# Kernel optimization log

Hardware: AMD Instinct MI355X
Metric: run time of the kernel (lower is better)

The kernel has to match this reference:

```python
import jax, jax.numpy as jnp
import numpy as np

EPS = 1e-7
NUM_HEADS = 16

def _ln(x, g, b):
    m = jnp.mean(x, -1, keepdims=True)
    v = jnp.var(x, -1, keepdims=True)
    return (x - m) * jax.lax.rsqrt(v + EPS) * g + b

def _gelu(x):
    return jax.nn.gelu(x, approximate=False)  # torch nn.GELU default = exact erf

def _attn(x, qkv_w, qkv_b, pw, pb):
    B, N, C = x.shape
    D = C // NUM_HEADS
    qkv = (x @ qkv_w.T + qkv_b).reshape(B, N, 3, NUM_HEADS, D).transpose(2, 0, 3, 1, 4)
    q, k, v = qkv[0], qkv[1], qkv[2]
    a = jax.nn.softmax(jnp.einsum('bhnd,bhmd->bhnm', q, k) * (D ** -0.5), axis=-1)
    o = jnp.einsum('bhnm,bhmd->bhnd', a, v).transpose(0, 2, 1, 3).reshape(B, N, C)
    return o @ pw.T + pb

def _gcn(x, w, b, adj):
    # x: (B,C,J); w: (C*K,C) 1x1 conv, then einsum 'nkctv,kvw->nctw' with t==1
    K = adj.shape[0]
    B, C, J = x.shape
    y = jnp.einsum('bcj,oc->boj', x, w) + b[None, :, None]
    y = y.reshape(B, K, C, J)
    return jnp.einsum('bkcv,kvw->bcw', y, adj)

def _mlp(x, w1, b1, w2, b2):
    return _gelu(_gelu(x @ w1.T + b1) @ w2.T + b2)

def _lrsc(x, adj, l1g, l1b, l2g, l2b, g1w, g1b, g2w, g2b, m1w, m1b, m2w, m2b):
    x = x.transpose(0, 2, 1)                       # (B,C,J)
    res = x
    xn = _ln(x, l1g, l1b)                          # LayerNorm over J
    x = res + _mlp(xn, m1w, m1b, m2w, m2b) + _gcn(xn, g1w, g1b, adj)
    x = _ln(x.transpose(0, 2, 1), l2g, l2b).transpose(0, 2, 1)  # LayerNorm over C
    res = x
    x = res + _mlp(x, m1w, m1b, m2w, m2b) + _gcn(x, g2w, g2b, adj)
    return x.transpose(0, 2, 1)                    # (B,J,C)

def _gkpc(x, lg, lb, q1w, q1b, p1w, p1b, q2w, q2b, p2w, p2b):
    x = x + _attn(_ln(x, lg, lb), q1w, q1b, p1w, p1b)
    return _attn(_ln(x, lg, lb), q2w, q2b, p2w, p2b)  # note: no residual on second attn

def _forward(x, adj, ln1_g, ln1_b, ln2_g, ln2_b, gcn1_w, gcn1_b, gcn2_w, gcn2_b,
             mlp1_w1, mlp1_b1, mlp1_w2, mlp1_b2, attn_ln_g, attn_ln_b,
             qkv1_w, qkv1_b, proj1_w, proj1_b, qkv2_w, qkv2_b, proj2_w, proj2_b,
             tn_g, tn_b):
    L = ln1_g.shape[0]
    for i in range(L):
        # GG_ACM/RR_ACM/LCM are published as identity -> both 0.3/0.7 mixes equal x + gelu(x)
        xin = x + _gelu(x)
        x5 = _gkpc(xin, attn_ln_g[i], attn_ln_b[i], qkv1_w[i], qkv1_b[i],
                   proj1_w[i], proj1_b[i], qkv2_w[i], qkv2_b[i], proj2_w[i], proj2_b[i])
        x7 = _lrsc(xin, adj, ln1_g[i], ln1_b[i], ln2_g[i], ln2_b[i],
                   gcn1_w[i], gcn1_b[i], gcn2_w[i], gcn2_b[i],
                   mlp1_w1[i], mlp1_b1[i], mlp1_w2[i], mlp1_b2[i])
        x = x + x5 + x7
    return _ln(x, tn_g, tn_b)

def setup_inputs():
    B, V, C, K, L = 2048, 17, 512, 3, 3
    s = 0.05
    ks = jax.random.split(jax.random.key(0), 12)
    rn = lambda k, sh: jax.random.normal(k, sh, jnp.float32) * s
    return dict(
        x=jax.random.normal(ks[0], (B, V, C), jnp.float32),
        adj=jax.random.uniform(ks[1], (K, V, V), dtype=jnp.float32),
        ln1_g=jnp.ones((L, V), jnp.float32), ln1_b=jnp.zeros((L, V), jnp.float32),
        ln2_g=jnp.ones((L, C), jnp.float32), ln2_b=jnp.zeros((L, C), jnp.float32),
        gcn1_w=rn(ks[2], (L, C * K, C)), gcn1_b=jnp.zeros((L, C * K), jnp.float32),
        gcn2_w=rn(ks[3], (L, C * K, C)), gcn2_b=jnp.zeros((L, C * K), jnp.float32),
        mlp1_w1=rn(ks[4], (L, C, V)), mlp1_b1=jnp.zeros((L, C), jnp.float32),
        mlp1_w2=rn(ks[5], (L, V, C)), mlp1_b2=jnp.zeros((L, V), jnp.float32),
        attn_ln_g=jnp.ones((L, C), jnp.float32), attn_ln_b=jnp.zeros((L, C), jnp.float32),
        qkv1_w=rn(ks[6], (L, 3 * C, C)), qkv1_b=jnp.zeros((L, 3 * C), jnp.float32),
        proj1_w=rn(ks[7], (L, C, C)), proj1_b=jnp.zeros((L, C), jnp.float32),
        qkv2_w=rn(ks[8], (L, 3 * C, C)), qkv2_b=jnp.zeros((L, 3 * C), jnp.float32),
        proj2_w=rn(ks[9], (L, C, C)), proj2_b=jnp.zeros((L, C), jnp.float32),
        tn_g=jnp.ones((C,), jnp.float32), tn_b=jnp.zeros((C,), jnp.float32),
    )

def reference(x, adj, ln1_g, ln1_b, ln2_g, ln2_b, gcn1_w, gcn1_b, gcn2_w, gcn2_b,
              mlp1_w1, mlp1_b1, mlp1_w2, mlp1_b2, attn_ln_g, attn_ln_b,
              qkv1_w, qkv1_b, proj1_w, proj1_b, qkv2_w, qkv2_b, proj2_w, proj2_b,
              tn_g, tn_b):
    return _forward(x, adj, ln1_g, ln1_b, ln2_g, ln2_b, gcn1_w, gcn1_b, gcn2_w, gcn2_b,
                    mlp1_w1, mlp1_b1, mlp1_w2, mlp1_b2, attn_ln_g, attn_ln_b,
                    qkv1_w, qkv1_b, proj1_w, proj1_b, qkv2_w, qkv2_b, proj2_w, proj2_b,
                    tn_g, tn_b)
```

## Files before the change

### kernel.cpp

```cpp
#include <hip/hip_runtime.h>
#include <hip/hip_bf16.h>
#include <math.h>

#define Bn 2048
#define Vn 17
#define Cn 512
static const size_t NE = (size_t)Bn * Vn * Cn;
#define MROWS (Bn * Vn)

typedef __attribute__((ext_vector_type(8))) short bf16x8;
typedef __attribute__((ext_vector_type(4))) short bf16x4;
typedef __attribute__((ext_vector_type(4))) float f32x4;
typedef __attribute__((ext_vector_type(2))) unsigned int u32x2;
typedef unsigned short u16;

__device__ __forceinline__ float u2f(u16 u) { return __uint_as_float(((unsigned)u) << 16); }
__device__ __forceinline__ u16 f2u(float f) {
    unsigned u = __float_as_uint(f);
    return (u16)((u + 0x7fffu + ((u >> 16) & 1u)) >> 16);
}
__device__ __forceinline__ float gelu_f(float x) {
    return 0.5f * x * (1.0f + erff(x * 0.70710678118654752f));
}
__device__ __forceinline__ float exp2_raw(float x) {
    float r; asm("v_exp_f32 %0, %1" : "=v"(r) : "v"(x)); return r;
}
__device__ __forceinline__ float gelu_fast(float x) {
    float b = x * fmaf(x * x, -0.10294348f, -2.30220820f);
    return x * __builtin_amdgcn_rcpf(1.0f + exp2_raw(b));
}
__device__ __forceinline__ unsigned cvtpk(float lo, float hi) {
    unsigned r; asm("v_cvt_pk_bf16_f32 %0, %1, %2" : "=v"(r) : "v"(lo), "v"(hi)); return r;
}
__device__ __forceinline__ bf16x4 gelupk(f32x4 v) {
    u32x2 t = {cvtpk(gelu_fast(v[0]), gelu_fast(v[1])), cvtpk(gelu_fast(v[2]), gelu_fast(v[3]))};
    return __builtin_bit_cast(bf16x4, t);
}
__device__ __forceinline__ f32x4 mfma16(bf16x4 a, bf16x4 b, f32x4 c) {
    asm("v_mfma_f32_16x16x16_bf16 %0, %1, %2, %0" : "+v"(c) : "v"(a), "v"(b));
    return c;
}
__device__ __forceinline__ void gload16(const u16* g, u16* l) {
    __builtin_amdgcn_global_load_lds((const __attribute__((address_space(1))) void*)g,
                                     (__attribute__((address_space(3))) void*)l, 16, 0, 0);
}

__global__ void k_diag(float* __restrict__ o, float v, int n) {
    int i = blockIdx.x * 256 + threadIdx.x;
    if (i < n) o[i] = v;
}

__global__ void k_f2b(const float4* __restrict__ s, ushort4* __restrict__ d, int n4) {
    int i = blockIdx.x * 256 + threadIdx.x;
    if (i >= n4) return;
    float4 v = s[i];
    ushort4 o = {f2u(v.x), f2u(v.y), f2u(v.z), f2u(v.w)};
    d[i] = o;
}

__global__ void k_mpad(const float* __restrict__ W1, const float* __restrict__ W2,
                       u16* __restrict__ W1p, u16* __restrict__ W2p) {
    int t = blockIdx.x * 256 + threadIdx.x;
    if (t < 512 * 32) {
        int o = t >> 5, j = t & 31;
        W1p[t] = (j < 17) ? f2u(W1[o * 17 + j]) : (u16)0;
    } else {
        int t2 = t - 512 * 32;
        int w = t2 >> 9;
        W2p[t2] = (w < 17) ? f2u(W2[t2]) : (u16)0;
    }
}

__global__ void k_xingelu(const float* __restrict__ X, u16* __restrict__ O, int n8) {
    int i = blockIdx.x * 256 + threadIdx.x;
    if (i >= n8) return;
    float4 a = *(const float4*)(X + (size_t)i * 8);
    float4 b = *(const float4*)(X + (size_t)i * 8 + 4);
    float v[8] = {a.x, a.y, a.z, a.w, b.x, b.y, b.z, b.w};
    bf16x8 r;
#pragma unroll
    for (int k = 0; k < 8; k++) r[k] = f2u(v[k] + gelu_f(v[k]));
    *(bf16x8*)(O + (size_t)i * 8) = r;
}

template <int F32IO>
__global__ __launch_bounds__(256) void k_ln_c(const void* __restrict__ Xv,
                                              const float* __restrict__ g,
                                              const float* __restrict__ bt,
                                              void* __restrict__ Ov, int nrows) {
    int row = blockIdx.x * 4 + (threadIdx.x >> 6);
    if (row >= nrows) return;
    int lane = threadIdx.x & 63;
    float vv[8];
    if (F32IO) {
        const float* xp = (const float*)Xv + (size_t)row * Cn + lane * 8;
        float4 v0 = *(const float4*)xp, v1 = *(const float4*)(xp + 4);
        vv[0] = v0.x; vv[1] = v0.y; vv[2] = v0.z; vv[3] = v0.w;
        vv[4] = v1.x; vv[5] = v1.y; vv[6] = v1.z; vv[7] = v1.w;
    } else {
        bf16x8 h = *(const bf16x8*)((const u16*)Xv + (size_t)row * Cn + lane * 8);
#pragma unroll
        for (int k = 0; k < 8; k++) vv[k] = u2f((u16)h[k]);
    }
    float s = 0.f, q = 0.f;
#pragma unroll
    for (int k = 0; k < 8; k++) { s += vv[k]; q = fmaf(vv[k], vv[k], q); }
#pragma unroll
    for (int o = 32; o; o >>= 1) { s += __shfl_xor(s, o); q += __shfl_xor(q, o); }
    float mean = s * (1.f / Cn);
    float var = q * (1.f / Cn) - mean * mean;
    float inv = 1.f / sqrtf(var + 1e-7f);
    int cb = lane * 8;
    if (F32IO) {
        float r[8];
#pragma unroll
        for (int k = 0; k < 8; k++) r[k] = (vv[k] - mean) * inv * g[cb + k] + bt[cb + k];
        float* op = (float*)Ov + (size_t)row * Cn + cb;
        *(float4*)op = make_float4(r[0], r[1], r[2], r[3]);
        *(float4*)(op + 4) = make_float4(r[4], r[5], r[6], r[7]);
    } else {
        bf16x8 r;
#pragma unroll
        for (int k = 0; k < 8; k++) r[k] = f2u((vv[k] - mean) * inv * g[cb + k] + bt[cb + k]);
        *(bf16x8*)((u16*)Ov + (size_t)row * Cn + cb) = r;
    }
}

__global__ __launch_bounds__(256) void k_ln_j(const u16* __restrict__ X,
                                              const float* __restrict__ g,
                                              const float* __restrict__ bt,
                                              u16* __restrict__ O) {
    int idx = blockIdx.x * 256 + threadIdx.x;
    int b = idx >> 9, c = idx & 511;
    const u16* xp = X + (size_t)b * Vn * Cn + c;
    float v[Vn];
    float s = 0.f;
#pragma unroll
    for (int j = 0; j < Vn; j++) { v[j] = u2f(xp[(size_t)j * Cn]); s += v[j]; }
    float mean = s * (1.f / Vn);
    float q = 0.f;
#pragma unroll
    for (int j = 0; j < Vn; j++) { float d = v[j] - mean; q = fmaf(d, d, q); }
    float inv = 1.f / sqrtf(q * (1.f / Vn) + 1e-7f);
    u16* op = O + (size_t)b * Vn * Cn + c;
#pragma unroll
    for (int j = 0; j < Vn; j++) op[(size_t)j * Cn] = f2u((v[j] - mean) * inv * g[j] + bt[j]);
}

template <int REMAP, int EPI>
__global__ __launch_bounds__(256) void k_gemm(const u16* __restrict__ A, const u16* __restrict__ W,
                                              const float* __restrict__ bias, u16* __restrict__ OutB,
                                              const u16* __restrict__ Res, float* __restrict__ Xf,
                                              int hbase, int shift) {
    constexpr int NT = REMAP ? 6 : 8;
    const int K = 512;
    int wave = threadIdx.x >> 6, lane = threadIdx.x & 63;
    int m0 = blockIdx.x * 128 + wave * 32;
    int nbase = blockIdx.y * (16 * NT);
    int r16 = lane & 15, kq = lane >> 4;
    int ld = REMAP ? (3 << shift) : 512;

    const u16* wp[NT];
    int wrow[NT];
#pragma unroll
    for (int nt = 0; nt < NT; nt++) {
        int n = nbase + nt * 16 + r16;
        int wr;
        if (REMAP) {
            int s = n >> shift, off = n & ((1 << shift) - 1);
            wr = (s << 9) + hbase + off;
        } else wr = n;
        wrow[nt] = wr;
        wp[nt] = W + (size_t)wr * K + kq * 8;
    }
    f32x4 acc[2][NT];
#pragma unroll
    for (int i = 0; i < 2; i++)
#pragma unroll
        for (int nt = 0; nt < NT; nt++) acc[i][nt] = (f32x4){0.f, 0.f, 0.f, 0.f};

    const u16* ap = A + (size_t)(m0 + r16) * K + kq * 8;
    for (int k0 = 0; k0 < K; k0 += 32) {
        bf16x8 a0 = *(const bf16x8*)(ap + k0);
        bf16x8 a1 = *(const bf16x8*)(ap + (size_t)16 * K + k0);
#pragma unroll
        for (int nt = 0; nt < NT; nt++) {
            bf16x8 bf = *(const bf16x8*)(wp[nt] + k0);
            acc[0][nt] = __builtin_amdgcn_mfma_f32_16x16x32_bf16(a0, bf, acc[0][nt], 0, 0, 0);
            acc[1][nt] = __builtin_amdgcn_mfma_f32_16x16x32_bf16(a1, bf, acc[1][nt], 0, 0, 0);
        }
    }
#pragma unroll
    for (int nt = 0; nt < NT; nt++) {
        float bv = bias[wrow[nt]];
        int n = nbase + nt * 16 + r16;
#pragma unroll
        for (int i = 0; i < 2; i++) {
#pragma unroll
            for (int r = 0; r < 4; r++) {
                size_t mb = (size_t)(m0 + i * 16 + kq * 4 + r);
                float v = acc[i][nt][r] + bv;
                if (EPI == 0) OutB[mb * ld + n] = f2u(v);
                else if (EPI == 1) { size_t o = mb * 512 + n; OutB[o] = f2u(v + u2f(Res[o])); }
                else { size_t o = mb * 512 + n; Xf[o] += v; }
            }
        }
    }
}

template <int EPI, int NY>
__global__ __launch_bounds__(256) void k_gemm2(const u16* __restrict__ A, const u16* __restrict__ W,
                                               const float* __restrict__ bias, u16* __restrict__ OutB,
                                               const u16* __restrict__ Res, float* __restrict__ Xf,
                                               int N) {
    __shared__ u16 As[128 * 64];
    __shared__ u16 Bs[128 * 64];
    const int K = 512;
    int tid = threadIdx.x;
    int wave = tid >> 6, lane = tid & 63;
    int cpx = gridDim.x >> 3;
    int bid = blockIdx.x;
    int swz = (bid & 7) * cpx + (bid >> 3);
    int m0 = (swz / NY) * 128, n0 = (swz % NY) * 128;
    int r16 = lane & 15, kq = lane >> 4;

    int srow = wave << 2;
    int lrow = lane >> 3;
    int lcol = (lane & 7) * 8;

    f32x4 acc[2][8];
#pragma unroll
    for (int i = 0; i < 2; i++)
#pragma unroll
        for (int j = 0; j < 8; j++) acc[i][j] = (f32x4){0.f, 0.f, 0.f, 0.f};

    const u16* aT = As + (wave * 32 + r16) * 64 + kq * 8;
    const u16* bT = Bs + r16 * 64 + kq * 8;

    for (int k0 = 0; k0 < K; k0 += 64) {
#pragma unroll
        for (int i = 0; i < 4; i++) {
            int rows = (srow + i) * 8 + lrow;
            gload16(A + (size_t)(m0 + rows) * K + k0 + lcol, (u16*)As + (srow + i) * 512);
            gload16(W + (size_t)(n0 + rows) * K + k0 + lcol, (u16*)Bs + (srow + i) * 512);
        }
        __syncthreads();
#pragma unroll
        for (int kk = 0; kk < 64; kk += 32) {
            bf16x8 af0 = *(const bf16x8*)(aT + kk);
            bf16x8 af1 = *(const bf16x8*)(aT + 16 * 64 + kk);
#pragma unroll
            for (int nt = 0; nt < 8; nt++) {
                bf16x8 bf = *(const bf16x8*)(bT + nt * 16 * 64 + kk);
                acc[0][nt] = __builtin_amdgcn_mfma_f32_16x16x32_bf16(af0, bf, acc[0][nt], 0, 0, 0);
                acc[1][nt] = __builtin_amdgcn_mfma_f32_16x16x32_bf16(af1, bf, acc[1][nt], 0, 0, 0);
            }
        }
        __syncthreads();
    }

    int mw = m0 + wave * 32;
#pragma unroll
    for (int nt = 0; nt < 8; nt++) {
        int n = n0 + nt * 16 + r16;
        float bv = bias[n];
#pragma unroll
        for (int i = 0; i < 2; i++) {
#pragma unroll
            for (int r = 0; r < 4; r++) {
                size_t mb = (size_t)(mw + i * 16 + kq * 4 + r);
                size_t o = mb * N + n;
                float v = acc[i][nt][r] + bv;
                if (EPI == 0) OutB[o] = f2u(v);
                else if (EPI == 1) OutB[o] = f2u(v + u2f(Res[o]));
                else Xf[o] += v;
            }
        }
    }
}

__global__ __launch_bounds__(256) void k_attn(const u16* __restrict__ Y, u16* __restrict__ T,
                                              int shift, int hgbase, int l2ch) {
    int wv = threadIdx.x >> 6, lane = threadIdx.x & 63;
    if (lane >= 34) return;
    int gw = blockIdx.x * 4 + wv;
    int which = (lane >= 17) ? 1 : 0;
    int j = lane - which * 17;
    int pid = gw * 2 + which;
    int b = pid >> l2ch;
    int hl = pid & ((1 << l2ch) - 1);
    int CW = 1 << shift;
    int row3 = 3 << shift;

    const u16* qb = Y + (size_t)(b * Vn + j) * row3 + hl * 32;
    float q[32];
#pragma unroll
    for (int d0 = 0; d0 < 32; d0 += 8) {
        bf16x8 h = *(const bf16x8*)(qb + d0);
#pragma unroll
        for (int d = 0; d < 8; d++) q[d0 + d] = u2f((u16)h[d]);
    }
    float sc[Vn];
    float mx = -1e30f;
#pragma unroll
    for (int kk = 0; kk < Vn; kk++) {
        const u16* kb = Y + (size_t)(b * Vn + kk) * row3 + CW + hl * 32;
        float s = 0.f;
#pragma unroll
        for (int d0 = 0; d0 < 32; d0 += 8) {
            bf16x8 h = *(const bf16x8*)(kb + d0);
#pragma unroll
            for (int d = 0; d < 8; d++) s = fmaf(q[d0 + d], u2f((u16)h[d]), s);
        }
        s *= 0.1767766952966369f;
        sc[kk] = s;
        mx = fmaxf(mx, s);
    }
    float sum = 0.f;
#pragma unroll
    for (int kk = 0; kk < Vn; kk++) { sc[kk] = __expf(sc[kk] - mx); sum += sc[kk]; }
    float inv = 1.f / sum;
    float o[32];
#pragma unroll
    for (int d = 0; d < 32; d++) o[d] = 0.f;
#pragma unroll
    for (int kk = 0; kk < Vn; kk++) {
        const u16* vb = Y + (size_t)(b * Vn + kk) * row3 + 2 * CW + hl * 32;
        float p = sc[kk] * inv;
#pragma unroll
        for (int d0 = 0; d0 < 32; d0 += 8) {
            bf16x8 h = *(const bf16x8*)(vb + d0);
#pragma unroll
            for (int d = 0; d < 8; d++) o[d0 + d] = fmaf(p, u2f((u16)h[d]), o[d0 + d]);
        }
    }
    u16* op = T + (size_t)(b * Vn + j) * Cn + hgbase + hl * 32;
#pragma unroll
    for (int d0 = 0; d0 < 32; d0 += 8) {
        bf16x8 r;
#pragma unroll
        for (int d = 0; d < 8; d++) r[d] = f2u(o[d0 + d]);
        *(bf16x8*)(op + d0) = r;
    }
}

template <int MODE>
__global__ __launch_bounds__(256) void k_agg(const u16* __restrict__ Y, const float* __restrict__ Adj,
                                             const u16* __restrict__ aux1, const u16* __restrict__ aux2,
                                             u16* __restrict__ OutB, float* __restrict__ Xf,
                                             int cbase, int shift) {
    __shared__ float adj_s[3][Vn][Vn];
    for (int t = threadIdx.x; t < 3 * Vn * Vn; t += 256) {
        int k = t / (Vn * Vn), r = t - k * Vn * Vn;
        adj_s[k][r / Vn][r % Vn] = Adj[t];
    }
    __syncthreads();
    int CW = 1 << shift;
    int idx = blockIdx.x * 256 + threadIdx.x;
    int b = idx >> shift, co = idx & (CW - 1);
    int c = cbase + co;
    int row3 = 3 << shift;
    float acc[Vn];
#pragma unroll
    for (int w = 0; w < Vn; w++) acc[w] = 0.f;
    const u16* yb = Y + (size_t)b * Vn * row3 + co;
#pragma unroll
    for (int k = 0; k < 3; k++)
#pragma unroll
        for (int v = 0; v < Vn; v++) {
            float y = u2f(yb[(size_t)v * row3 + k * CW]);
#pragma unroll
            for (int w = 0; w < Vn; w++) acc[w] = fmaf(y, adj_s[k][v][w], acc[w]);
        }
    size_t rb = (size_t)(b * Vn) * Cn + c;
#pragma unroll
    for (int w = 0; w < Vn; w++) {
        size_t o = rb + (size_t)w * Cn;
        float val = acc[w] + u2f(aux1[o]) + u2f(aux2[o]);
        if (MODE == 0) OutB[o] = f2u(val);
        else Xf[o] += val;
    }
}

__global__ __launch_bounds__(512) void k_mlp(const u16* __restrict__ X,
                                             const u16* __restrict__ W1p, const float* __restrict__ B1,
                                             const u16* __restrict__ W2p, const float* __restrict__ B2,
                                             u16* __restrict__ O) {
    __shared__ u16 Xs[256 * 40];
    __shared__ float B1s[512];
    int b = blockIdx.x >> 1;
    int cbase = (blockIdx.x & 1) << 8;
    int tid = threadIdx.x;

    for (int i = tid; i < 256 * 40 / 8; i += 512) ((float4*)Xs)[i] = make_float4(0.f, 0.f, 0.f, 0.f);
    if (tid < 128) ((float4*)B1s)[tid] = ((const float4*)B1)[tid];
    __syncthreads();
    const u16* xb = X + (size_t)b * (Vn * Cn) + cbase;
    for (int i = tid; i < 17 * 256; i += 512) {
        int j = i >> 8, c = i & 255;
        Xs[c * 40 + j] = xb[j * Cn + c];
    }
    __syncthreads();

    int wave = tid >> 6, lane = tid & 63;
    int r16 = lane & 15, kq = lane >> 4;
    int crow = wave * 32;

    bf16x8 xf0 = *(const bf16x8*)(Xs + (crow + r16) * 40 + kq * 8);
    bf16x8 xf1 = *(const bf16x8*)(Xs + (crow + 16 + r16) * 40 + kq * 8);

    f32x4 acc2[2][2];
#pragma unroll
    for (int i = 0; i < 2; i++)
#pragma unroll
        for (int j = 0; j < 2; j++) acc2[i][j] = (f32x4){0.f, 0.f, 0.f, 0.f};

    for (int s = 0; s < 16; s++) {
        const u16* w1p = W1p + ((s * 32 + r16) << 5) + kq * 8;
        bf16x8 af0 = *(const bf16x8*)w1p;
        bf16x8 af1 = *(const bf16x8*)(w1p + 16 * 32);
        f32x4 bi0 = *(const f32x4*)(B1s + s * 32 + kq * 4);
        f32x4 bi1 = *(const f32x4*)(B1s + s * 32 + 16 + kq * 4);
        f32x4 a00 = __builtin_amdgcn_mfma_f32_16x16x32_bf16(af0, xf0, bi0, 0, 0, 0);
        f32x4 a01 = __builtin_amdgcn_mfma_f32_16x16x32_bf16(af0, xf1, bi0, 0, 0, 0);
        f32x4 a10 = __builtin_amdgcn_mfma_f32_16x16x32_bf16(af1, xf0, bi1, 0, 0, 0);
        f32x4 a11 = __builtin_amdgcn_mfma_f32_16x16x32_bf16(af1, xf1, bi1, 0, 0, 0);
        bf16x4 p00 = gelupk(a00);
        bf16x4 p01 = gelupk(a01);
        bf16x4 p10 = gelupk(a10);
        bf16x4 p11 = gelupk(a11);
        const u16* w2p = W2p + (size_t)r16 * 512 + s * 32 + kq * 4;
        bf16x4 wb00 = *(const bf16x4*)(w2p);
        bf16x4 wb01 = *(const bf16x4*)(w2p + 16);
        bf16x4 wb10 = *(const bf16x4*)(w2p + 16 * 512);
        bf16x4 wb11 = *(const bf16x4*)(w2p + 16 * 512 + 16);
        acc2[0][0] = mfma16(p00, wb00, acc2[0][0]);
        acc2[0][0] = mfma16(p10, wb01, acc2[0][0]);
        acc2[1][0] = mfma16(p01, wb00, acc2[1][0]);
        acc2[1][0] = mfma16(p11, wb01, acc2[1][0]);
        acc2[0][1] = mfma16(p00, wb10, acc2[0][1]);
        acc2[0][1] = mfma16(p10, wb11, acc2[0][1]);
        acc2[1][1] = mfma16(p01, wb10, acc2[1][1]);
        acc2[1][1] = mfma16(p11, wb11, acc2[1][1]);
    }

    u16* ob = O + (size_t)b * (Vn * Cn) + cbase;
    float bb0 = B2[r16];
#pragma unroll
    for (int cg = 0; cg < 2; cg++) {
        int cl = crow + cg * 16 + kq * 4;
        f32x4 v = acc2[cg][0];
        uint2 pk = make_uint2(cvtpk(gelu_fast(v[0] + bb0), gelu_fast(v[1] + bb0)),
                              cvtpk(gelu_fast(v[2] + bb0), gelu_fast(v[3] + bb0)));
        *(uint2*)(ob + (size_t)r16 * Cn + cl) = pk;
        if (r16 == 0) {
            float bb1 = B2[16];
            f32x4 w = acc2[cg][1];
            uint2 pk1 = make_uint2(cvtpk(gelu_fast(w[0] + bb1), gelu_fast(w[1] + bb1)),
                                   cvtpk(gelu_fast(w[2] + bb1), gelu_fast(w[3] + bb1)));
            *(uint2*)(ob + (size_t)16 * Cn + cl) = pk1;
        }
    }
}

extern "C" void kernel_launch(void* const* d_in, const int* in_sizes, int n_in,
                              void* d_out, int out_size, void* d_ws, size_t ws_size,
                              hipStream_t stream) {
    (void)in_sizes; (void)n_in; (void)out_size;
    typedef const float* fp;
    fp x_in = (fp)d_in[0];
    fp adj = (fp)d_in[1];
    fp ln1_g = (fp)d_in[2], ln1_b = (fp)d_in[3];
    fp ln2_g = (fp)d_in[4], ln2_b = (fp)d_in[5];
    fp gcn1_w = (fp)d_in[6], gcn1_b = (fp)d_in[7];
    fp gcn2_w = (fp)d_in[8], gcn2_b = (fp)d_in[9];
    fp m1w = (fp)d_in[10], m1b = (fp)d_in[11];
    fp m2w = (fp)d_in[12], m2b = (fp)d_in[13];
    fp aln_g = (fp)d_in[14], aln_b = (fp)d_in[15];
    fp qkv1_w = (fp)d_in[16], qkv1_b = (fp)d_in[17];
    fp p1w = (fp)d_in[18], p1b = (fp)d_in[19];
    fp qkv2_w = (fp)d_in[20], qkv2_b = (fp)d_in[21];
    fp p2w = (fp)d_in[22], p2b = (fp)d_in[23];
    fp tn_g = (fp)d_in[24], tn_b = (fp)d_in[25];

    const size_t NE2 = NE * 2;
    const size_t WSCR_SZ = (size_t)1536 * 512 * 2;
    const size_t MPAD_SZ = (size_t)(512 * 32 + 32 * 512) * 2;

    int CH = 0;
    for (int ch = 16; ch >= 1; ch >>= 1) {
        size_t need = 3 * NE2 + WSCR_SZ + MPAD_SZ + (size_t)MROWS * 96 * ch * 2 + 1024;
        if (need <= ws_size) { CH = ch; break; }
    }
    if (!CH) {
        k_diag<<<(int)((NE + 255) / 256), 256, 0, stream>>>((float*)d_out, (float)ws_size, (int)NE);
        return;
    }
    const int l2ch = __builtin_ctz(CH);
    const int shift = 5 + l2ch;
    const int NCH = 16 / CH;
    const bool FAST = (CH == 16);

    char* p = (char*)d_ws;
    u16* XIN = (u16*)p;  p += NE2;
    u16* T1 = (u16*)p;   p += NE2;
    u16* T2 = (u16*)p;   p += NE2;
    u16* YCH = (u16*)p;  p += (size_t)MROWS * 96 * CH * 2;
    u16* WSCR = (u16*)p; p += WSCR_SZ;
    u16* MPAD1 = (u16*)p;
    u16* MPAD2 = MPAD1 + 512 * 32;

    float* X = (float*)d_out;
    hipMemcpyAsync(X, x_in, NE * 4, hipMemcpyDeviceToDevice, stream);

    const int G8 = (int)(NE / 8 / 256);
    const int GLN = MROWS / 4;
    const int GBC = Bn * Cn / 256;
    const int GATT = (Bn << l2ch) / 8;
    const int GAGG = (Bn << shift) / 256;
    const dim3 GEMM_C(MROWS / 128, CH);
    const dim3 GEMM_P(MROWS / 128, 4);
    const int CV_QKV = (int)(1536 * 512 / 4 / 256);
    const int CV_P = (int)(512 * 512 / 4 / 256);
    const int GQF = (MROWS / 128) * 12;
    const int GPF = (MROWS / 128) * 4;

    for (int i = 0; i < 3; i++) {
        fp q1w = qkv1_w + (size_t)i * 1536 * 512, q1b = qkv1_b + i * 1536;
        fp q2w = qkv2_w + (size_t)i * 1536 * 512, q2b = qkv2_b + i * 1536;
        fp g1w = gcn1_w + (size_t)i * 1536 * 512, g1b = gcn1_b + i * 1536;
        fp g2w = gcn2_w + (size_t)i * 1536 * 512, g2b = gcn2_b + i * 1536;
        fp pw1 = p1w + (size_t)i * 512 * 512, pb1 = p1b + i * Cn;
        fp pw2 = p2w + (size_t)i * 512 * 512, pb2 = p2b + i * Cn;
        fp alg = aln_g + i * Cn, alb = aln_b + i * Cn;
        fp l1g = ln1_g + i * Vn, l1b_ = ln1_b + i * Vn;
        fp l2g = ln2_g + i * Cn, l2b_ = ln2_b + i * Cn;
        fp w1 = m1w + (size_t)i * Cn * Vn, b1 = m1b + i * Cn;
        fp w2 = m2w + (size_t)i * Vn * Cn, b2 = m2b + i * Vn;

        k_xingelu<<<G8, 256, 0, stream>>>(X, XIN, (int)(NE / 8));
        k_mpad<<<128, 256, 0, stream>>>(w1, w2, MPAD1, MPAD2);

        k_ln_c<0><<<GLN, 256, 0, stream>>>(XIN, alg, alb, T1, MROWS);
        k_f2b<<<CV_QKV, 256, 0, stream>>>((const float4*)q1w, (ushort4*)WSCR, 1536 * 512 / 4);
        if (FAST) {
            k_gemm2<0, 12><<<GQF, 256, 0, stream>>>(T1, WSCR, q1b, YCH, nullptr, nullptr, 1536);
            k_attn<<<GATT, 256, 0, stream>>>(YCH, T2, shift, 0, l2ch);
        } else {
            for (int hg = 0; hg < NCH; hg++) {
                k_gemm<1, 0><<<GEMM_C, 256, 0, stream>>>(T1, WSCR, q1b, YCH, nullptr, nullptr, hg << shift, shift);
                k_attn<<<GATT, 256, 0, stream>>>(YCH, T2, shift, hg << shift, l2ch);
            }
        }
        k_f2b<<<CV_P, 256, 0, stream>>>((const float4*)pw1, (ushort4*)WSCR, 512 * 512 / 4);
        if (FAST) k_gemm2<1, 4><<<GPF, 256, 0, stream>>>(T2, WSCR, pb1, T1, XIN, nullptr, 512);
        else k_gemm<0, 1><<<GEMM_P, 256, 0, stream>>>(T2, WSCR, pb1, T1, XIN, nullptr, 0, 0);
        k_ln_c<0><<<GLN, 256, 0, stream>>>(T1, alg, alb, T2, MROWS);
        k_f2b<<<CV_QKV, 256, 0, stream>>>((const float4*)q2w, (ushort4*)WSCR, 1536 * 512 / 4);
        if (FAST) {
            k_gemm2<0, 12><<<GQF, 256, 0, stream>>>(T2, WSCR, q2b, YCH, nullptr, nullptr, 1536);
            k_attn<<<GATT, 256, 0, stream>>>(YCH, T1, shift, 0, l2ch);
        } else {
            for (int hg = 0; hg < NCH; hg++) {
                k_gemm<1, 0><<<GEMM_C, 256, 0, stream>>>(T2, WSCR, q2b, YCH, nullptr, nullptr, hg << shift, shift);
                k_attn<<<GATT, 256, 0, stream>>>(YCH, T1, shift, hg << shift, l2ch);
            }
        }
        k_f2b<<<CV_P, 256, 0, stream>>>((const float4*)pw2, (ushort4*)WSCR, 512 * 512 / 4);
        if (FAST) k_gemm2<2, 4><<<GPF, 256, 0, stream>>>(T1, WSCR, pb2, nullptr, nullptr, X, 512);
        else k_gemm<0, 2><<<GEMM_P, 256, 0, stream>>>(T1, WSCR, pb2, nullptr, nullptr, X, 0, 0);

        k_ln_j<<<GBC, 256, 0, stream>>>(XIN, l1g, l1b_, T1);
        k_mlp<<<Bn * 2, 512, 0, stream>>>(T1, MPAD1, b1, MPAD2, b2, T2);
        k_f2b<<<CV_QKV, 256, 0, stream>>>((const float4*)g1w, (ushort4*)WSCR, 1536 * 512 / 4);
        if (FAST) {
            k_gemm2<0, 12><<<GQF, 256, 0, stream>>>(T1, WSCR, g1b, YCH, nullptr, nullptr, 1536);
            k_agg<0><<<GAGG, 256, 0, stream>>>(YCH, adj, XIN, T2, XIN, nullptr, 0, shift);
        } else {
            for (int cc = 0; cc < NCH; cc++) {
                k_gemm<1, 0><<<GEMM_C, 256, 0, stream>>>(T1, WSCR, g1b, YCH, nullptr, nullptr, cc << shift, shift);
                k_agg<0><<<GAGG, 256, 0, stream>>>(YCH, adj, XIN, T2, XIN, nullptr, cc << shift, shift);
            }
        }
        k_ln_c<0><<<GLN, 256, 0, stream>>>(XIN, l2g, l2b_, T1, MROWS);
        k_mlp<<<Bn * 2, 512, 0, stream>>>(T1, MPAD1, b1, MPAD2, b2, T2);
        k_f2b<<<CV_QKV, 256, 0, stream>>>((const float4*)g2w, (ushort4*)WSCR, 1536 * 512 / 4);
        if (FAST) {
            k_gemm2<0, 12><<<GQF, 256, 0, stream>>>(T1, WSCR, g2b, YCH, nullptr, nullptr, 1536);
            k_agg<1><<<GAGG, 256, 0, stream>>>(YCH, adj, T1, T2, nullptr, X, 0, shift);
        } else {
            for (int cc = 0; cc < NCH; cc++) {
                k_gemm<1, 0><<<GEMM_C, 256, 0, stream>>>(T1, WSCR, g2b, YCH, nullptr, nullptr, cc << shift, shift);
                k_agg<1><<<GAGG, 256, 0, stream>>>(YCH, adj, T1, T2, nullptr, X, cc << shift, shift);
            }
        }
    }

    k_ln_c<1><<<GLN, 256, 0, stream>>>(X, tn_g, tn_b, X, MROWS);
}
```

Before: 4.397 ms.

## Pre-convert all layer weights upfront and stage MLP hidden via LDS

When the workspace is large enough, all per-layer weights are converted to bf16 in one batch at the start instead of re-converting into a shared scratch before every GEMM. This removes many small conversion launches from the per-layer sequence. The MLP kernel now writes GELU outputs to an LDS buffer and reloads them as 16x16x32 MFMA operands, replacing the 16x16x16 inline-asm MFMAs. Inline-asm exp and bf16 packing are swapped for builtins. The cost is extra workspace and extra LDS per block.

Result: faster. 3.774 ms (-14.2%).

```diff
diff --git a/kernel.cpp b/kernel.cpp
--- a/kernel.cpp
+++ b/kernel.cpp
@@ -9,9 +9,7 @@
 #define MROWS (Bn * Vn)
 
 typedef __attribute__((ext_vector_type(8))) short bf16x8;
-typedef __attribute__((ext_vector_type(4))) short bf16x4;
 typedef __attribute__((ext_vector_type(4))) float f32x4;
-typedef __attribute__((ext_vector_type(2))) unsigned int u32x2;
 typedef unsigned short u16;
 
 __device__ __forceinline__ float u2f(u16 u) { return __uint_as_float(((unsigned)u) << 16); }
@@ -22,23 +20,22 @@
 __device__ __forceinline__ float gelu_f(float x) {
     return 0.5f * x * (1.0f + erff(x * 0.70710678118654752f));
 }
-__device__ __forceinline__ float exp2_raw(float x) {
-    float r; asm("v_exp_f32 %0, %1" : "=v"(r) : "v"(x)); return r;
+__device__ __forceinline__ float exp2f_fast(float b) {
+#if __has_builtin(__builtin_amdgcn_exp2f)
+    return __builtin_amdgcn_exp2f(b);
+#else
+    return __expf(b * 0.69314718056f);
+#endif
 }
 __device__ __forceinline__ float gelu_fast(float x) {
     float b = x * fmaf(x * x, -0.10294348f, -2.30220820f);
-    return x * __builtin_amdgcn_rcpf(1.0f + exp2_raw(b));
-}
-__device__ __forceinline__ unsigned cvtpk(float lo, float hi) {
-    unsigned r; asm("v_cvt_pk_bf16_f32 %0, %1, %2" : "=v"(r) : "v"(lo), "v"(hi)); return r;
-}
-__device__ __forceinline__ bf16x4 gelupk(f32x4 v) {
-    u32x2 t = {cvtpk(gelu_fast(v[0]), gelu_fast(v[1])), cvtpk(gelu_fast(v[2]), gelu_fast(v[3]))};
-    return __builtin_bit_cast(bf16x4, t);
-}
-__device__ __forceinline__ f32x4 mfma16(bf16x4 a, bf16x4 b, f32x4 c) {
-    asm("v_mfma_f32_16x16x16_bf16 %0, %1, %2, %0" : "+v"(c) : "v"(a), "v"(b));
-    return c;
+    return x * __builtin_amdgcn_rcpf(1.0f + exp2f_fast(b));
+}
+__device__ __forceinline__ unsigned pk2(float lo, float hi) {
+    __hip_bfloat162 h = __float22bfloat162_rn(make_float2(lo, hi));
+    unsigned r;
+    __builtin_memcpy(&r, &h, 4);
+    return r;
 }
 __device__ __forceinline__ void gload16(const u16* g, u16* l) {
     __builtin_amdgcn_global_load_lds((const __attribute__((address_space(1))) void*)g,
@@ -387,6 +384,7 @@
                                              const u16* __restrict__ W2p, const float* __restrict__ B2,
                                              u16* __restrict__ O) {
     __shared__ u16 Xs[256 * 40];
+    __shared__ u16 Hs[256 * 40];
     __shared__ float B1s[512];
     int b = blockIdx.x >> 1;
     int cbase = (blockIdx.x & 1) << 8;
@@ -414,6 +412,8 @@
     for (int i = 0; i < 2; i++)
 #pragma unroll
         for (int j = 0; j < 2; j++) acc2[i][j] = (f32x4){0.f, 0.f, 0.f, 0.f};
+
+    const u16* hs0 = Hs + (crow + r16) * 40 + kq * 8;
 
     for (int s = 0; s < 16; s++) {
         const u16* w1p = W1p + ((s * 32 + r16) << 5) + kq * 8;
@@ -425,40 +425,44 @@
         f32x4 a01 = __builtin_amdgcn_mfma_f32_16x16x32_bf16(af0, xf1, bi0, 0, 0, 0);
         f32x4 a10 = __builtin_amdgcn_mfma_f32_16x16x32_bf16(af1, xf0, bi1, 0, 0, 0);
         f32x4 a11 = __builtin_amdgcn_mfma_f32_16x16x32_bf16(af1, xf1, bi1, 0, 0, 0);
-        bf16x4 p00 = gelupk(a00);
-        bf16x4 p01 = gelupk(a01);
-        bf16x4 p10 = gelupk(a10);
-        bf16x4 p11 = gelupk(a11);
-        const u16* w2p = W2p + (size_t)r16 * 512 + s * 32 + kq * 4;
-        bf16x4 wb00 = *(const bf16x4*)(w2p);
-        bf16x4 wb01 = *(const bf16x4*)(w2p + 16);
-        bf16x4 wb10 = *(const bf16x4*)(w2p + 16 * 512);
-        bf16x4 wb11 = *(const bf16x4*)(w2p + 16 * 512 + 16);
-        acc2[0][0] = mfma16(p00, wb00, acc2[0][0]);
-        acc2[0][0] = mfma16(p10, wb01, acc2[0][0]);
-        acc2[1][0] = mfma16(p01, wb00, acc2[1][0]);
-        acc2[1][0] = mfma16(p11, wb01, acc2[1][0]);
-        acc2[0][1] = mfma16(p00, wb10, acc2[0][1]);
-        acc2[0][1] = mfma16(p10, wb11, acc2[0][1]);
-        acc2[1][1] = mfma16(p01, wb10, acc2[1][1]);
-        acc2[1][1] = mfma16(p11, wb11, acc2[1][1]);
+#define STORE_H(ACC, NT, OT)                                                             \
+        {                                                                                 \
+            unsigned g0 = pk2(gelu_fast(ACC[0]), gelu_fast(ACC[1]));                      \
+            unsigned g1 = pk2(gelu_fast(ACC[2]), gelu_fast(ACC[3]));                      \
+            *(uint2*)(Hs + (crow + NT * 16 + r16) * 40 + OT * 16 + kq * 4) =              \
+                make_uint2(g0, g1);                                                       \
+        }
+        STORE_H(a00, 0, 0)
+        STORE_H(a01, 1, 0)
+        STORE_H(a10, 0, 1)
+        STORE_H(a11, 1, 1)
+#undef STORE_H
+        __builtin_amdgcn_sched_barrier(0);
+        bf16x8 h0 = *(const bf16x8*)hs0;
+        bf16x8 h1 = *(const bf16x8*)(hs0 + 16 * 40);
+        const u16* w2p = W2p + s * 32 + kq * 8;
+        bf16x8 wf0 = *(const bf16x8*)(w2p + r16 * 512);
+        bf16x8 wf1 = *(const bf16x8*)(w2p + 16 * 512);
+        acc2[0][0] = __builtin_amdgcn_mfma_f32_16x16x32_bf16(h0, wf0, acc2[0][0], 0, 0, 0);
+        acc2[0][1] = __builtin_amdgcn_mfma_f32_16x16x32_bf16(h0, wf1, acc2[0][1], 0, 0, 0);
+        acc2[1][0] = __builtin_amdgcn_mfma_f32_16x16x32_bf16(h1, wf0, acc2[1][0], 0, 0, 0);
+        acc2[1][1] = __builtin_amdgcn_mfma_f32_16x16x32_bf16(h1, wf1, acc2[1][1], 0, 0, 0);
     }
 
     u16* ob = O + (size_t)b * (Vn * Cn) + cbase;
-    float bb0 = B2[r16];
-#pragma unroll
-    for (int cg = 0; cg < 2; cg++) {
-        int cl = crow + cg * 16 + kq * 4;
-        f32x4 v = acc2[cg][0];
-        uint2 pk = make_uint2(cvtpk(gelu_fast(v[0] + bb0), gelu_fast(v[1] + bb0)),
-                              cvtpk(gelu_fast(v[2] + bb0), gelu_fast(v[3] + bb0)));
-        *(uint2*)(ob + (size_t)r16 * Cn + cl) = pk;
-        if (r16 == 0) {
-            float bb1 = B2[16];
-            f32x4 w = acc2[cg][1];
-            uint2 pk1 = make_uint2(cvtpk(gelu_fast(w[0] + bb1), gelu_fast(w[1] + bb1)),
-                                   cvtpk(gelu_fast(w[2] + bb1), gelu_fast(w[3] + bb1)));
-            *(uint2*)(ob + (size_t)16 * Cn + cl) = pk1;
+#pragma unroll
+    for (int nt = 0; nt < 2; nt++) {
+        int cl = crow + nt * 16 + kq * 4;
+#pragma unroll
+        for (int n2 = 0; n2 < 2; n2++) {
+            int w = n2 * 16 + r16;
+            if (w < 17) {
+                float bb = B2[w];
+                f32x4 v = acc2[nt][n2];
+                uint2 pk = make_uint2(pk2(gelu_fast(v[0] + bb), gelu_fast(v[1] + bb)),
+                                      pk2(gelu_fast(v[2] + bb), gelu_fast(v[3] + bb)));
+                *(uint2*)(ob + (size_t)w * Cn + cl) = pk;
+            }
         }
     }
 }
@@ -484,13 +488,22 @@
     fp tn_g = (fp)d_in[24], tn_b = (fp)d_in[25];
 
     const size_t NE2 = NE * 2;
+    const size_t YCH16 = (size_t)MROWS * 96 * 16 * 2;
+    const size_t SZ_QKV3 = (size_t)3 * 1536 * 512;
+    const size_t SZ_P3 = (size_t)3 * 512 * 512;
+    const size_t MPADL = (size_t)(512 * 32 + 32 * 512);
+    const size_t POOLB = (4 * SZ_QKV3 + 2 * SZ_P3 + 3 * MPADL) * 2;
     const size_t WSCR_SZ = (size_t)1536 * 512 * 2;
-    const size_t MPAD_SZ = (size_t)(512 * 32 + 32 * 512) * 2;
-
+    const size_t MPAD_SZ = MPADL * 2;
+
+    bool FULLW = false;
     int CH = 0;
-    for (int ch = 16; ch >= 1; ch >>= 1) {
-        size_t need = 3 * NE2 + WSCR_SZ + MPAD_SZ + (size_t)MROWS * 96 * ch * 2 + 1024;
-        if (need <= ws_size) { CH = ch; break; }
+    if (3 * NE2 + YCH16 + POOLB + 1024 <= ws_size) { FULLW = true; CH = 16; }
+    else {
+        for (int ch = 16; ch >= 1; ch >>= 1) {
+            size_t need = 3 * NE2 + WSCR_SZ + MPAD_SZ + (size_t)MROWS * 96 * ch * 2 + 1024;
+            if (need <= ws_size) { CH = ch; break; }
+        }
     }
     if (!CH) {
         k_diag<<<(int)((NE + 255) / 256), 256, 0, stream>>>((float*)d_out, (float)ws_size, (int)NE);
@@ -506,12 +519,37 @@
     u16* T1 = (u16*)p;   p += NE2;
     u16* T2 = (u16*)p;   p += NE2;
     u16* YCH = (u16*)p;  p += (size_t)MROWS * 96 * CH * 2;
-    u16* WSCR = (u16*)p; p += WSCR_SZ;
-    u16* MPAD1 = (u16*)p;
-    u16* MPAD2 = MPAD1 + 512 * 32;
+    u16 *WQ1 = nullptr, *WQ2 = nullptr, *WG1 = nullptr, *WG2 = nullptr,
+        *WP1 = nullptr, *WP2 = nullptr, *MP1 = nullptr, *MP2 = nullptr, *WSCR = nullptr;
+    if (FULLW) {
+        WQ1 = (u16*)p; p += SZ_QKV3 * 2;
+        WQ2 = (u16*)p; p += SZ_QKV3 * 2;
+        WG1 = (u16*)p; p += SZ_QKV3 * 2;
+        WG2 = (u16*)p; p += SZ_QKV3 * 2;
+        WP1 = (u16*)p; p += SZ_P3 * 2;
+        WP2 = (u16*)p; p += SZ_P3 * 2;
+        MP1 = (u16*)p; p += 3 * 16384 * 2;
+        MP2 = (u16*)p; p += 3 * 16384 * 2;
+    } else {
+        WSCR = (u16*)p; p += WSCR_SZ;
+        MP1 = (u16*)p;  p += 16384 * 2;
+        MP2 = (u16*)p;
+    }
 
     float* X = (float*)d_out;
-    hipMemcpyAsync(X, x_in, NE * 4, hipMemcpyDeviceToDevice, stream);
+    (void)hipMemcpyAsync(X, x_in, NE * 4, hipMemcpyDeviceToDevice, stream);
+
+    if (FULLW) {
+        k_f2b<<<2304, 256, 0, stream>>>((const float4*)qkv1_w, (ushort4*)WQ1, (int)(SZ_QKV3 / 4));
+        k_f2b<<<2304, 256, 0, stream>>>((const float4*)qkv2_w, (ushort4*)WQ2, (int)(SZ_QKV3 / 4));
+        k_f2b<<<2304, 256, 0, stream>>>((const float4*)gcn1_w, (ushort4*)WG1, (int)(SZ_QKV3 / 4));
+        k_f2b<<<2304, 256, 0, stream>>>((const float4*)gcn2_w, (ushort4*)WG2, (int)(SZ_QKV3 / 4));
+        k_f2b<<<768, 256, 0, stream>>>((const float4*)p1w, (ushort4*)WP1, (int)(SZ_P3 / 4));
+        k_f2b<<<768, 256, 0, stream>>>((const float4*)p2w, (ushort4*)WP2, (int)(SZ_P3 / 4));
+        for (int l = 0; l < 3; l++)
+            k_mpad<<<128, 256, 0, stream>>>(m1w + (size_t)l * Cn * Vn, m2w + (size_t)l * Vn * Cn,
+                                            MP1 + l * 16384, MP2 + l * 16384);
+    }
 
     const int G8 = (int)(NE / 8 / 256);
     const int GLN = MROWS / 4;
@@ -538,13 +576,22 @@
         fp w1 = m1w + (size_t)i * Cn * Vn, b1 = m1b + i * Cn;
         fp w2 = m2w + (size_t)i * Vn * Cn, b2 = m2b + i * Vn;
 
+        const u16* wq1p = FULLW ? WQ1 + (size_t)i * 1536 * 512 : WSCR;
+        const u16* wq2p = FULLW ? WQ2 + (size_t)i * 1536 * 512 : WSCR;
+        const u16* wg1p = FULLW ? WG1 + (size_t)i * 1536 * 512 : WSCR;
+        const u16* wg2p = FULLW ? WG2 + (size_t)i * 1536 * 512 : WSCR;
+        const u16* wp1p = FULLW ? WP1 + (size_t)i * 512 * 512 : WSCR;
+        const u16* wp2p = FULLW ? WP2 + (size_t)i * 512 * 512 : WSCR;
+        const u16* mp1 = FULLW ? MP1 + i * 16384 : MP1;
+        const u16* mp2 = FULLW ? MP2 + i * 16384 : MP2;
+
         k_xingelu<<<G8, 256, 0, stream>>>(X, XIN, (int)(NE / 8));
-        k_mpad<<<128, 256, 0, stream>>>(w1, w2, MPAD1, MPAD2);
+        if (!FULLW) k_mpad<<<128, 256, 0, stream>>>(w1, w2, (u16*)mp1, (u16*)mp2);
 
         k_ln_c<0><<<GLN, 256, 0, stream>>>(XIN, alg, alb, T1, MROWS);
-        k_f2b<<<CV_QKV, 256, 0, stream>>>((const float4*)q1w, (ushort4*)WSCR, 1536 * 512 / 4);
+        if (!FULLW) k_f2b<<<CV_QKV, 256, 0, stream>>>((const float4*)q1w, (ushort4*)WSCR, 1536 * 512 / 4);
         if (FAST) {
-            k_gemm2<0, 12><<<GQF, 256, 0, stream>>>(T1, WSCR, q1b, YCH, nullptr, nullptr, 1536);
+            k_gemm2<0, 12><<<GQF, 256, 0, stream>>>(T1, wq1p, q1b, YCH, nullptr, nullptr, 1536);
             k_attn<<<GATT, 256, 0, stream>>>(YCH, T2, shift, 0, l2ch);
         } else {
             for (int hg = 0; hg < NCH; hg++) {
@@ -552,13 +599,13 @@
                 k_attn<<<GATT, 256, 0, stream>>>(YCH, T2, shift, hg << shift, l2ch);
             }
         }
-        k_f2b<<<CV_P, 256, 0, stream>>>((const float4*)pw1, (ushort4*)WSCR, 512 * 512 / 4);
-        if (FAST) k_gemm2<1, 4><<<GPF, 256, 0, stream>>>(T2, WSCR, pb1, T1, XIN, nullptr, 512);
+        if (!FULLW) k_f2b<<<CV_P, 256, 0, stream>>>((const float4*)pw1, (ushort4*)WSCR, 512 * 512 / 4);
+        if (FAST) k_gemm2<1, 4><<<GPF, 256, 0, stream>>>(T2, wp1p, pb1, T1, XIN, nullptr, 512);
         else k_gemm<0, 1><<<GEMM_P, 256, 0, stream>>>(T2, WSCR, pb1, T1, XIN, nullptr, 0, 0);
         k_ln_c<0><<<GLN, 256, 0, stream>>>(T1, alg, alb, T2, MROWS);
-        k_f2b<<<CV_QKV, 256, 0, stream>>>((const float4*)q2w, (ushort4*)WSCR, 1536 * 512 / 4);
+        if (!FULLW) k_f2b<<<CV_QKV, 256, 0, stream>>>((const float4*)q2w, (ushort4*)WSCR, 1536 * 512 / 4);
         if (FAST) {
-            k_gemm2<0, 12><<<GQF, 256, 0, stream>>>(T2, WSCR, q2b, YCH, nullptr, nullptr, 1536);
+            k_gemm2<0, 12><<<GQF, 256, 0, stream>>>(T2, wq2p, q2b, YCH, nullptr, nullptr, 1536);
             k_attn<<<GATT, 256, 0, stream>>>(YCH, T1, shift, 0, l2ch);
         } else {
             for (int hg = 0; hg < NCH; hg++) {
@@ -566,15 +613,15 @@
                 k_attn<<<GATT, 256, 0, stream>>>(YCH, T1, shift, hg << shift, l2ch);
             }
         }
-        k_f2b<<<CV_P, 256, 0, stream>>>((const float4*)pw2, (ushort4*)WSCR, 512 * 512 / 4);
-        if (FAST) k_gemm2<2, 4><<<GPF, 256, 0, stream>>>(T1, WSCR, pb2, nullptr, nullptr, X, 512);
+        if (!FULLW) k_f2b<<<CV_P, 256, 0, stream>>>((const float4*)pw2, (ushort4*)WSCR, 512 * 512 / 4);
+        if (FAST) k_gemm2<2, 4><<<GPF, 256, 0, stream>>>(T1, wp2p, pb2, nullptr, nullptr, X, 512);
         else k_gemm<0, 2><<<GEMM_P, 256, 0, stream>>>(T1, WSCR, pb2, nullptr, nullptr, X, 0, 0);
 
         k_ln_j<<<GBC, 256, 0, stream>>>(XIN, l1g, l1b_, T1);
-        k_mlp<<<Bn * 2, 512, 0, stream>>>(T1, MPAD1, b1, MPAD2, b2, T2);
-        k_f2b<<<CV_QKV, 256, 0, stream>>>((const float4*)g1w, (ushort4*)WSCR, 1536 * 512 / 4);
+        k_mlp<<<Bn * 2, 512, 0, stream>>>(T1, mp1, b1, mp2, b2, T2);
+        if (!FULLW) k_f2b<<<CV_QKV, 256, 0, stream>>>((const float4*)g1w, (ushort4*)WSCR, 1536 * 512 / 4);
         if (FAST) {
-            k_gemm2<0, 12><<<GQF, 256, 0, stream>>>(T1, WSCR, g1b, YCH, nullptr, nullptr, 1536);
+            k_gemm2<0, 12><<<GQF, 256, 0, stream>>>(T1, wg1p, g1b, YCH, nullptr, nullptr, 1536);
             k_agg<0><<<GAGG, 256, 0, stream>>>(YCH, adj, XIN, T2, XIN, nullptr, 0, shift);
         } else {
             for (int cc = 0; cc < NCH; cc++) {
@@ -583,10 +630,10 @@
             }
         }
         k_ln_c<0><<<GLN, 256, 0, stream>>>(XIN, l2g, l2b_, T1, MROWS);
-        k_mlp<<<Bn * 2, 512, 0, stream>>>(T1, MPAD1, b1, MPAD2, b2, T2);
-        k_f2b<<<CV_QKV, 256, 0, stream>>>((const float4*)g2w, (ushort4*)WSCR, 1536 * 512 / 4);
+        k_mlp<<<Bn * 2, 512, 0, stream>>>(T1, mp1, b1, mp2, b2, T2);
+        if (!FULLW) k_f2b<<<CV_QKV, 256, 0, stream>>>((const float4*)g2w, (ushort4*)WSCR, 1536 * 512 / 4);
         if (FAST) {
-            k_gemm2<0, 12><<<GQF, 256, 0, stream>>>(T1, WSCR, g2b, YCH, nullptr, nullptr, 1536);
+            k_gemm2<0, 12><<<GQF, 256, 0, stream>>>(T1, wg2p, g2b, YCH, nullptr, nullptr, 1536);
             k_agg<1><<<GAGG, 256, 0, stream>>>(YCH, adj, T1, T2, nullptr, X, 0, shift);
         } else {
             for (int cc = 0; cc < NCH; cc++) {
```
